# Performance work log

Measured on AMD Instinct MI355X. Metric: run time of the kernel, lower is better.

The kernel has to match this reference:

```python
import jax, jax.numpy as jnp
import numpy as np

D, NH, NL, NP, NLAYERS = 256, 8, 4, 4, 6
DH = D // NH
SHAPES = [(76, 100), (38, 50), (19, 25), (10, 13)]
STARTS = [int(s) for s in np.cumsum([0] + [h * w for h, w in SHAPES])[:-1]]
LQ = sum(h * w for h, w in SHAPES)
B = 2


def _layernorm(x, g, b, eps=1e-5):
    m = x.mean(-1, keepdims=True)
    v = ((x - m) ** 2).mean(-1, keepdims=True)
    return (x - m) * jax.lax.rsqrt(v + eps) * g + b


def _ref_points():
    pts = []
    for H, W in SHAPES:
        ry = (jnp.arange(H, dtype=jnp.float32) + 0.5) / H
        rx = (jnp.arange(W, dtype=jnp.float32) + 0.5) / W
        gy, gx = jnp.meshgrid(ry, rx, indexing='ij')
        pts.append(jnp.stack([gx.ravel(), gy.ravel()], -1))
    ref = jnp.concatenate(pts, 0)  # [LQ, 2] (x, y)
    return jnp.broadcast_to(ref[:, None, :], (LQ, NL, 2))


def _bilinear(v, loc, H, W):
    # v: [BN, H*W, DH]; loc: [BN, N, 2] normalized (x, y).
    # Matches torch grid_sample(align_corners=False, padding='zeros') with grid=2*loc-1.
    px = loc[..., 0] * W - 0.5
    py = loc[..., 1] * H - 0.5
    x0f = jnp.floor(px)
    y0f = jnp.floor(py)
    lx = px - x0f
    ly = py - y0f
    x0 = x0f.astype(jnp.int32)
    y0 = y0f.astype(jnp.int32)
    out = jnp.zeros(loc.shape[:-1] + (DH,), v.dtype)
    for dy, dx, w in ((0, 0, (1 - ly) * (1 - lx)), (0, 1, (1 - ly) * lx), (1, 0, ly * (1 - lx)), (1, 1, ly * lx)):
        xi = x0 + dx
        yi = y0 + dy
        valid = (xi >= 0) & (xi < W) & (yi >= 0) & (yi < H)
        idx = jnp.clip(yi, 0, H - 1) * W + jnp.clip(xi, 0, W - 1)
        g = jnp.take_along_axis(v, idx[..., None], axis=1)  # [BN, N, DH]
        out = out + g * (w * valid)[..., None]
    return out


def _layer(src, pos, ref, p):
    q = src + pos
    value = (src @ p['w_val'] + p['b_val']).reshape(B, LQ, NH, DH)
    off = (q @ p['w_off'] + p['b_off']).reshape(B, LQ, NH, NL, NP, 2)
    aw = jax.nn.softmax((q @ p['w_attn'] + p['b_attn']).reshape(B, LQ, NH, NL * NP), -1)
    aw = aw.reshape(B, LQ, NH, NL, NP)
    norm = jnp.array([[w, h] for h, w in SHAPES], jnp.float32)  # [NL, 2] = (W, H)
    loc = ref[None, :, None, :, None, :] + off / norm[None, None, None, :, None, :]  # [B,LQ,NH,NL,NP,2]
    v_t = value.transpose(0, 2, 1, 3).reshape(B * NH, LQ, DH)
    out = jnp.zeros((B, NH, LQ, DH), src.dtype)
    for l, (H, W) in enumerate(SHAPES):
        vl = v_t[:, STARTS[l]:STARTS[l] + H * W]
        locl = loc[:, :, :, l].transpose(0, 2, 1, 3, 4).reshape(B * NH, LQ * NP, 2)
        g = _bilinear(vl, locl, H, W).reshape(B, NH, LQ, NP, DH)
        out = out + jnp.einsum('bhqp,bhqpd->bhqd', aw[:, :, :, l].transpose(0, 2, 1, 3), g)
    attn = out.transpose(0, 2, 1, 3).reshape(B, LQ, D) @ p['w_out'] + p['b_out']
    src = _layernorm(src + attn, p['ln1_g'], p['ln1_b'])
    ffn = jax.nn.relu(src @ p['w_ffn1'] + p['b_ffn1']) @ p['w_ffn2'] + p['b_ffn2']
    return _layernorm(src + ffn, p['ln2_g'], p['ln2_b'])


def setup_inputs() -> dict:
    key = jax.random.key(0)
    ks = jax.random.split(key, 16)
    inp = {}
    for i, (H, W) in enumerate(SHAPES):
        inp[f'src{i}'] = jax.random.normal(ks[i], (B, D, H, W), jnp.float32)
        inp[f'pos{i}'] = jax.random.normal(ks[4 + i], (B, D, H, W), jnp.float32)
    inp['level_embed'] = jax.random.normal(ks[8], (NL, D), jnp.float32)
    s = 0.02
    inp['w_off'] = jax.random.normal(ks[9], (NLAYERS, D, NH * NL * NP * 2), jnp.float32) * s
    inp['b_off'] = jnp.zeros((NLAYERS, NH * NL * NP * 2), jnp.float32)
    inp['w_attn'] = jax.random.normal(ks[10], (NLAYERS, D, NH * NL * NP), jnp.float32) * s
    inp['b_attn'] = jnp.zeros((NLAYERS, NH * NL * NP), jnp.float32)
    inp['w_val'] = jax.random.normal(ks[11], (NLAYERS, D, D), jnp.float32) * s
    inp['b_val'] = jnp.zeros((NLAYERS, D), jnp.float32)
    inp['w_out'] = jax.random.normal(ks[12], (NLAYERS, D, D), jnp.float32) * s
    inp['b_out'] = jnp.zeros((NLAYERS, D), jnp.float32)
    inp['ln1_g'] = jnp.ones((NLAYERS, D), jnp.float32)
    inp['ln1_b'] = jnp.zeros((NLAYERS, D), jnp.float32)
    inp['w_ffn1'] = jax.random.normal(ks[13], (NLAYERS, D, 1024), jnp.float32) * s
    inp['b_ffn1'] = jnp.zeros((NLAYERS, 1024), jnp.float32)
    inp['w_ffn2'] = jax.random.normal(ks[14], (NLAYERS, 1024, D), jnp.float32) * s
    inp['b_ffn2'] = jnp.zeros((NLAYERS, D), jnp.float32)
    inp['ln2_g'] = jnp.ones((NLAYERS, D), jnp.float32)
    inp['ln2_b'] = jnp.zeros((NLAYERS, D), jnp.float32)
    return inp


def reference(src0, src1, src2, src3, pos0, pos1, pos2, pos3, level_embed,
              w_off, b_off, w_attn, b_attn, w_val, b_val, w_out, b_out,
              ln1_g, ln1_b, w_ffn1, b_ffn1, w_ffn2, b_ffn2, ln2_g, ln2_b):
    srcs = [src0, src1, src2, src3]
    poss = [pos0, pos1, pos2, pos3]
    src_flat = jnp.concatenate(
        [s.reshape(B, D, -1).transpose(0, 2, 1) + level_embed[l][None, None] for l, s in enumerate(srcs)], 1)
    pos_flat = jnp.concatenate([p.reshape(B, D, -1).transpose(0, 2, 1) for p in poss], 1)
    ref = _ref_points()
    x = src_flat
    for i in range(NLAYERS):
        p = dict(w_off=w_off[i], b_off=b_off[i], w_attn=w_attn[i], b_attn=b_attn[i],
                 w_val=w_val[i], b_val=b_val[i], w_out=w_out[i], b_out=b_out[i],
                 ln1_g=ln1_g[i], ln1_b=ln1_b[i], w_ffn1=w_ffn1[i], b_ffn1=b_ffn1[i],
                 w_ffn2=w_ffn2[i], b_ffn2=b_ffn2[i], ln2_g=ln2_g[i], ln2_b=ln2_b[i])
        x = _layer(x, pos_flat, ref, p)
    return x  # [B, LQ, D] encoded memory
```

## Files before the change

kernel.cpp:

```cpp
#include <hip/hip_runtime.h>
#include <math.h>

#define LQ 10105
#define BATCH 2
#define NLAYERS 6
#define NTOK (BATCH * LQ)

typedef __attribute__((ext_vector_type(8))) short bf16x8;
typedef __attribute__((ext_vector_type(4))) float f32x4;

__device__ inline unsigned short f2bf_rne(float f) {
    unsigned u = __float_as_uint(f);
    unsigned r = u + 0x7fffu + ((u >> 16) & 1u);
    return (unsigned short)(r >> 16);
}
__device__ inline float bf2f(unsigned short h) {
    return __uint_as_float((unsigned)h << 16);
}

__global__ __launch_bounds__(256)
void flatten_k(const float* __restrict__ src, const float* __restrict__ pos,
               const float* __restrict__ lvl, float* __restrict__ src_flat,
               float* __restrict__ pos_flat, int HW, int start)
{
    int hw = blockIdx.x;
    int b  = blockIdx.y;
    int d  = threadIdx.x;
    float sv = src[((size_t)b * 256 + d) * HW + hw];
    float pv = pos[((size_t)b * 256 + d) * HW + hw];
    size_t o = ((size_t)(b * LQ + start + hw)) * 256 + d;
    src_flat[o] = sv + lvl[d];
    pos_flat[o] = pv;
}

__global__ __launch_bounds__(256)
void wsplit_k(const float* __restrict__ W, unsigned short* __restrict__ Th,
              unsigned short* __restrict__ Tl, int K, int N,
              long srcStride, long dstStride)
{
    __shared__ float t[32][33];
    int layer = blockIdx.z;
    int n0 = blockIdx.x * 32, k0 = blockIdx.y * 32;
    int tx = threadIdx.x & 31, ty = threadIdx.x >> 5;
    const float* Wsrc = W + (size_t)layer * srcStride;
    #pragma unroll
    for (int i = 0; i < 4; ++i)
        t[ty + i * 8][tx] = Wsrc[(size_t)(k0 + ty + i * 8) * N + n0 + tx];
    __syncthreads();
    unsigned short* th = Th + (size_t)layer * dstStride;
    unsigned short* tl = Tl + (size_t)layer * dstStride;
    #pragma unroll
    for (int i = 0; i < 4; ++i) {
        int n = n0 + ty + i * 8;
        float v = t[tx][ty + i * 8];
        unsigned short h = f2bf_rne(v);
        th[(size_t)n * K + k0 + tx] = h;
        tl[(size_t)n * K + k0 + tx] = f2bf_rne(v - bf2f(h));
    }
}

__global__ void boa_k(const float* __restrict__ b_off,
                      const float* __restrict__ b_attn, float* __restrict__ boa)
{
    int l = blockIdx.x, t = threadIdx.x;
    boa[l * 384 + t] = (t < 256) ? b_off[l * 256 + t] : b_attn[l * 128 + (t - 256)];
}

template<bool A_BF16, bool HAS_A2, bool RELU, bool HAS_RES, bool C_BF16>
__global__ __launch_bounds__(256)
void gemm_mfma(const void* __restrict__ Av, const float* __restrict__ A2,
               const unsigned short* __restrict__ Bh,
               const unsigned short* __restrict__ Bl,
               const float* __restrict__ bias, const float* __restrict__ Res,
               void* __restrict__ Cv, int M, int N, int K, int NB)
{
    constexpr int LDR = 40;
    constexpr int PLANES = A_BF16 ? 3 : 4;
    __shared__ unsigned short sMem[PLANES * 128 * LDR];
    unsigned short* sBh = sMem;
    unsigned short* sBl = sMem + 128 * LDR;
    unsigned short* sAh = sMem + 2 * 128 * LDR;
    unsigned short* sAl = sMem + (PLANES - 1) * 128 * LDR;

    const int nwg = gridDim.x;
    const int bid = blockIdx.x;
    const int q8 = nwg >> 3, r8 = nwg & 7, xcd = bid & 7;
    const int work = (xcd < r8 ? xcd * (q8 + 1) : r8 * (q8 + 1) + (xcd - r8) * q8)
                     + (bid >> 3);
    const int mblk = work / NB;
    const int m0 = mblk * 128;
    const int n0 = (work - mblk * NB) * 128;

    const int tid = threadIdx.x;
    const int w  = tid >> 6;
    const int l  = tid & 63;
    const int wm = (w >> 1) * 64;
    const int wn = (w & 1) * 64;
    const int lr = l & 15;
    const int kb = (l >> 4) * 8;
    const int rr = (l >> 4) * 4;

    const int sm = tid >> 1;
    const int sk = (tid & 1) * 16;
    const int arow = m0 + sm;
    const bool aok = arow < M;

    f32x4 acc[4][4];
    #pragma unroll
    for (int i = 0; i < 4; ++i)
        #pragma unroll
        for (int j = 0; j < 4; ++j)
            acc[i][j] = (f32x4){0.f, 0.f, 0.f, 0.f};

    for (int kt = 0; kt < K; kt += 32) {
        const unsigned short* bph = &Bh[(size_t)(n0 + sm) * K + kt + sk];
        const unsigned short* bpl = &Bl[(size_t)(n0 + sm) * K + kt + sk];
        bf16x8 vbh0 = *(const bf16x8*)(bph);
        bf16x8 vbh1 = *(const bf16x8*)(bph + 8);
        bf16x8 vbl0 = *(const bf16x8*)(bpl);
        bf16x8 vbl1 = *(const bf16x8*)(bpl + 8);

        bf16x8 ah0 = {}, ah1 = {}, al0 = {}, al1 = {};
        if constexpr (A_BF16) {
            if (aok) {
                const unsigned short* ap =
                    (const unsigned short*)Av + (size_t)arow * K + kt + sk;
                ah0 = *(const bf16x8*)ap;
                ah1 = *(const bf16x8*)(ap + 8);
            }
        } else {
            float va[16];
            if (aok) {
                const float* ap = (const float*)Av + (size_t)arow * K + kt + sk;
                *(float4*)&va[0]  = *(const float4*)(ap + 0);
                *(float4*)&va[4]  = *(const float4*)(ap + 4);
                *(float4*)&va[8]  = *(const float4*)(ap + 8);
                *(float4*)&va[12] = *(const float4*)(ap + 12);
                if (HAS_A2) {
                    const float* ap2 = &A2[(size_t)arow * K + kt + sk];
                    float4 t0 = *(const float4*)(ap2 + 0);
                    float4 t1 = *(const float4*)(ap2 + 4);
                    float4 t2 = *(const float4*)(ap2 + 8);
                    float4 t3 = *(const float4*)(ap2 + 12);
                    va[0] += t0.x; va[1] += t0.y; va[2]  += t0.z; va[3]  += t0.w;
                    va[4] += t1.x; va[5] += t1.y; va[6]  += t1.z; va[7]  += t1.w;
                    va[8] += t2.x; va[9] += t2.y; va[10] += t2.z; va[11] += t2.w;
                    va[12]+= t3.x; va[13]+= t3.y; va[14] += t3.z; va[15] += t3.w;
                }
            } else {
                #pragma unroll
                for (int j = 0; j < 16; ++j) va[j] = 0.f;
            }
            #pragma unroll
            for (int j = 0; j < 8; ++j) {
                float v0 = va[j], v1 = va[8 + j];
                unsigned short h0 = (unsigned short)(__float_as_uint(v0) >> 16);
                unsigned short h1 = (unsigned short)(__float_as_uint(v1) >> 16);
                ah0[j] = (short)h0;
                ah1[j] = (short)h1;
                float r0 = v0 - bf2f(h0);
                float r1 = v1 - bf2f(h1);
                al0[j] = (short)(unsigned short)(__float_as_uint(r0) >> 16);
                al1[j] = (short)(unsigned short)(__float_as_uint(r1) >> 16);
            }
        }

        __syncthreads();
        *(bf16x8*)&sAh[sm * LDR + sk]     = ah0;
        *(bf16x8*)&sAh[sm * LDR + sk + 8] = ah1;
        if constexpr (!A_BF16) {
            *(bf16x8*)&sAl[sm * LDR + sk]     = al0;
            *(bf16x8*)&sAl[sm * LDR + sk + 8] = al1;
        }
        *(bf16x8*)&sBh[sm * LDR + sk]     = vbh0;
        *(bf16x8*)&sBh[sm * LDR + sk + 8] = vbh1;
        *(bf16x8*)&sBl[sm * LDR + sk]     = vbl0;
        *(bf16x8*)&sBl[sm * LDR + sk + 8] = vbl1;
        __syncthreads();

        bf16x8 fah[4], fal[4];
        #pragma unroll
        for (int mf = 0; mf < 4; ++mf) {
            int off = (wm + mf * 16 + lr) * LDR + kb;
            fah[mf] = *(const bf16x8*)&sAh[off];
            if constexpr (!A_BF16) fal[mf] = *(const bf16x8*)&sAl[off];
        }
        #pragma unroll
        for (int nf = 0; nf < 4; ++nf) {
            int boff = (wn + nf * 16 + lr) * LDR + kb;
            bf16x8 fbh = *(const bf16x8*)&sBh[boff];
            bf16x8 fbl = *(const bf16x8*)&sBl[boff];
            #pragma unroll
            for (int mf = 0; mf < 4; ++mf) {
                f32x4 c = acc[mf][nf];
                c = __builtin_amdgcn_mfma_f32_16x16x32_bf16(fah[mf], fbh, c, 0, 0, 0);
                c = __builtin_amdgcn_mfma_f32_16x16x32_bf16(fah[mf], fbl, c, 0, 0, 0);
                if constexpr (!A_BF16)
                    c = __builtin_amdgcn_mfma_f32_16x16x32_bf16(fal[mf], fbh, c, 0, 0, 0);
                acc[mf][nf] = c;
            }
        }
    }

    float* Cf = (float*)Cv;
    unsigned short* Cb = (unsigned short*)Cv;
    #pragma unroll
    for (int nf = 0; nf < 4; ++nf) {
        int col = n0 + wn + nf * 16 + lr;
        float bs = bias[col];
        #pragma unroll
        for (int mf = 0; mf < 4; ++mf) {
            int rowb = m0 + wm + mf * 16 + rr;
            #pragma unroll
            for (int r = 0; r < 4; ++r) {
                int row = rowb + r;
                if (row < M) {
                    float v = acc[mf][nf][r] + bs;
                    if (HAS_RES) v += Res[(size_t)row * N + col];
                    if (RELU) v = fmaxf(v, 0.f);
                    if constexpr (C_BF16)
                        Cb[(size_t)row * N + col] = f2bf_rne(v);
                    else
                        Cf[(size_t)row * N + col] = v;
                }
            }
        }
    }
}

__global__ __launch_bounds__(256)
void sample_k(const unsigned short* __restrict__ val,
              const float* __restrict__ oab, unsigned short* __restrict__ out)
{
    const int Hs[4] = {76, 38, 19, 10};
    const int Ws[4] = {100, 50, 25, 13};
    const int ST[4] = {0, 7600, 9500, 9975};

    int bid = blockIdx.x;
    int xcd = bid & 7;
    const int qch = LQ >> 3;
    const int rem = LQ & 7;
    int q = (xcd < rem ? xcd * (qch + 1) : rem * (qch + 1) + (xcd - rem) * qch)
            + (bid >> 3);
    int b = blockIdx.y;
    int tid = threadIdx.x;

    __shared__ int2 s_iw[512];

    if (tid < 128) {
        int h = tid >> 4, pt = tid & 15, lvl = pt >> 2, p = pt & 3;
        int lq, local;
        if (q < 7600)      { lq = 0; local = q; }
        else if (q < 9500) { lq = 1; local = q - 7600; }
        else if (q < 9975) { lq = 2; local = q - 9500; }
        else               { lq = 3; local = q - 9975; }
        int Wq = Ws[lq], Hq = Hs[lq];
        int ry = local / Wq, rx = local - ry * Wq;
        float refx = (rx + 0.5f) / (float)Wq;
        float refy = (ry + 0.5f) / (float)Hq;

        size_t rowb = (size_t)(b * LQ + q) * 384;
        float logit = oab[rowb + 256 + h * 16 + pt];
        float mx = logit;
        mx = fmaxf(mx, __shfl_xor(mx, 1, 64));
        mx = fmaxf(mx, __shfl_xor(mx, 2, 64));
        mx = fmaxf(mx, __shfl_xor(mx, 4, 64));
        mx = fmaxf(mx, __shfl_xor(mx, 8, 64));
        float e = expf(logit - mx);
        float s = e;
        s += __shfl_xor(s, 1, 64);
        s += __shfl_xor(s, 2, 64);
        s += __shfl_xor(s, 4, 64);
        s += __shfl_xor(s, 8, 64);
        float aw = e / s;

        float ox = oab[rowb + h * 32 + lvl * 8 + p * 2];
        float oy = oab[rowb + h * 32 + lvl * 8 + p * 2 + 1];
        int W = Ws[lvl], H = Hs[lvl], st = ST[lvl];
        float px = refx * (float)W + ox - 0.5f;
        float py = refy * (float)H + oy - 0.5f;
        float x0f = floorf(px), y0f = floorf(py);
        float lx = px - x0f, ly = py - y0f;
        int x0 = (int)x0f, y0 = (int)y0f;
        int x1 = x0 + 1, y1 = y0 + 1;
        float ax0 = ((x0 >= 0) & (x0 < W)) ? (1.f - lx) : 0.f;
        float ax1 = ((x1 >= 0) & (x1 < W)) ? lx : 0.f;
        float ay0 = ((y0 >= 0) & (y0 < H)) ? (1.f - ly) : 0.f;
        float ay1 = ((y1 >= 0) & (y1 < H)) ? ly : 0.f;
        int cx0 = min(max(x0, 0), W - 1), cx1 = min(max(x1, 0), W - 1);
        int cy0 = min(max(y0, 0), H - 1), cy1 = min(max(y1, 0), H - 1);
        int i00 = st + cy0 * W + cx0, i01 = st + cy0 * W + cx1;
        int i10 = st + cy1 * W + cx0, i11 = st + cy1 * W + cx1;
        int base4 = tid * 4;
        s_iw[base4 + 0] = make_int2(i00, __float_as_int(aw * ay0 * ax0));
        s_iw[base4 + 1] = make_int2(i01, __float_as_int(aw * ay0 * ax1));
        s_iw[base4 + 2] = make_int2(i10, __float_as_int(aw * ay1 * ax0));
        s_iw[base4 + 3] = make_int2(i11, __float_as_int(aw * ay1 * ax1));
    }
    __syncthreads();

    int lane   = tid & 63;
    int wv     = tid >> 6;
    int h      = wv * 2 + (lane >> 5);
    int half   = lane & 31;
    int corner = half >> 3;
    int c4     = half & 7;
    const unsigned short* vb = val + (size_t)(b * LQ) * 256 + h * 32 + c4 * 4;
    int sbase = h * 64 + corner;

    float4 acc = make_float4(0.f, 0.f, 0.f, 0.f);
    #pragma unroll
    for (int pt = 0; pt < 16; ++pt) {
        int2 iw = s_iw[sbase + pt * 4];
        float wgt = __int_as_float(iw.y);
        ushort4 v = *(const ushort4*)&vb[(size_t)iw.x * 256];
        acc.x += wgt * bf2f(v.x); acc.y += wgt * bf2f(v.y);
        acc.z += wgt * bf2f(v.z); acc.w += wgt * bf2f(v.w);
    }
    acc.x += __shfl_xor(acc.x, 8, 64);  acc.y += __shfl_xor(acc.y, 8, 64);
    acc.z += __shfl_xor(acc.z, 8, 64);  acc.w += __shfl_xor(acc.w, 8, 64);
    acc.x += __shfl_xor(acc.x, 16, 64); acc.y += __shfl_xor(acc.y, 16, 64);
    acc.z += __shfl_xor(acc.z, 16, 64); acc.w += __shfl_xor(acc.w, 16, 64);

    if (corner == 0) {
        ushort4 o;
        o.x = f2bf_rne(acc.x); o.y = f2bf_rne(acc.y);
        o.z = f2bf_rne(acc.z); o.w = f2bf_rne(acc.w);
        *(ushort4*)&out[(size_t)(b * LQ + q) * 256 + h * 32 + c4 * 4] = o;
    }
}

__global__ __launch_bounds__(256)
void ln_k(const float* __restrict__ x, const float* __restrict__ g,
          const float* __restrict__ bt, float* __restrict__ out, int nrows)
{
    int row = blockIdx.x * 4 + (threadIdx.x >> 6);
    int lane = threadIdx.x & 63;
    if (row >= nrows) return;

    float4 v = *(const float4*)&x[(size_t)row * 256 + lane * 4];
    float s = v.x + v.y + v.z + v.w;
    #pragma unroll
    for (int o = 32; o > 0; o >>= 1) s += __shfl_down(s, o, 64);
    s = __shfl(s, 0, 64);
    float m = s * (1.0f / 256.0f);
    float cx = v.x - m, cy = v.y - m, cz = v.z - m, cw = v.w - m;
    float s2 = cx * cx + cy * cy + cz * cz + cw * cw;
    #pragma unroll
    for (int o = 32; o > 0; o >>= 1) s2 += __shfl_down(s2, o, 64);
    s2 = __shfl(s2, 0, 64);
    float rstd = rsqrtf(s2 * (1.0f / 256.0f) + 1e-5f);

    float4 gv = *(const float4*)&g[lane * 4];
    float4 bv = *(const float4*)&bt[lane * 4];
    float4 r;
    r.x = cx * rstd * gv.x + bv.x;
    r.y = cy * rstd * gv.y + bv.y;
    r.z = cz * rstd * gv.z + bv.z;
    r.w = cw * rstd * gv.w + bv.w;
    *(float4*)&out[(size_t)row * 256 + lane * 4] = r;
}

extern "C" void kernel_launch(void* const* d_in, const int* in_sizes, int n_in,
                              void* d_out, int out_size, void* d_ws, size_t ws_size,
                              hipStream_t stream)
{
    const float* src_in[4] = {(const float*)d_in[0], (const float*)d_in[2],
                              (const float*)d_in[4], (const float*)d_in[6]};
    const float* pos_in[4] = {(const float*)d_in[1], (const float*)d_in[3],
                              (const float*)d_in[5], (const float*)d_in[7]};
    const float* lvl    = (const float*)d_in[8];
    const float* w_off  = (const float*)d_in[9];
    const float* b_off  = (const float*)d_in[10];
    const float* w_attn = (const float*)d_in[11];
    const float* b_attn = (const float*)d_in[12];
    const float* w_val  = (const float*)d_in[13];
    const float* b_val  = (const float*)d_in[14];
    const float* w_out  = (const float*)d_in[15];
    const float* b_out  = (const float*)d_in[16];
    const float* ln1_g  = (const float*)d_in[17];
    const float* ln1_b  = (const float*)d_in[18];
    const float* w_ffn1 = (const float*)d_in[19];
    const float* b_ffn1 = (const float*)d_in[20];
    const float* w_ffn2 = (const float*)d_in[21];
    const float* b_ffn2 = (const float*)d_in[22];
    const float* ln2_g  = (const float*)d_in[23];
    const float* ln2_b  = (const float*)d_in[24];

    float* ws    = (float*)d_ws;
    float* src   = ws;
    float* pos   = src   + (size_t)NTOK * 256;
    float* preln = pos   + (size_t)NTOK * 256;
    char*  uni   = (char*)(preln + (size_t)NTOK * 256);
    unsigned short* valb = (unsigned short*)uni;
    float* oab = (float*)(uni + (size_t)NTOK * 512);
    unsigned short* samp = (unsigned short*)(uni + (size_t)NTOK * 2048);
    unsigned short* ffnb = (unsigned short*)uni;
    float* boa = (float*)(uni + (size_t)NTOK * 2560);
    unsigned short* Wh = (unsigned short*)(boa + 6 * 384);
    const long WL = 753664;
    unsigned short* Wl = Wh + (size_t)NLAYERS * WL;
    const long O_VAL = 0, O_OFF = 65536, O_ATT = 131072, O_OUT = 163840,
               O_F1 = 229376, O_F2 = 491520;

    wsplit_k<<<dim3(8, 8, 6),  256, 0, stream>>>(w_val,  Wh + O_VAL, Wl + O_VAL, 256, 256,  65536, WL);
    wsplit_k<<<dim3(8, 8, 6),  256, 0, stream>>>(w_off,  Wh + O_OFF, Wl + O_OFF, 256, 256,  65536, WL);
    wsplit_k<<<dim3(4, 8, 6),  256, 0, stream>>>(w_attn, Wh + O_ATT, Wl + O_ATT, 256, 128,  32768, WL);
    wsplit_k<<<dim3(8, 8, 6),  256, 0, stream>>>(w_out,  Wh + O_OUT, Wl + O_OUT, 256, 256,  65536, WL);
    wsplit_k<<<dim3(32, 8, 6), 256, 0, stream>>>(w_ffn1, Wh + O_F1,  Wl + O_F1,  256, 1024, 262144, WL);
    wsplit_k<<<dim3(8, 32, 6), 256, 0, stream>>>(w_ffn2, Wh + O_F2,  Wl + O_F2,  1024, 256, 262144, WL);
    boa_k<<<dim3(6), dim3(384), 0, stream>>>(b_off, b_attn, boa);

    const int HWs[4] = {7600, 1900, 475, 130};
    const int STt[4] = {0, 7600, 9500, 9975};
    for (int l = 0; l < 4; ++l) {
        dim3 g(HWs[l], BATCH);
        flatten_k<<<g, 256, 0, stream>>>(src_in[l], pos_in[l], lvl + l * 256,
                                         src, pos, HWs[l], STt[l]);
    }

    const int MB = (NTOK + 127) / 128;
    const int LNB = (NTOK + 3) / 4;
    dim3 blk(256);

    for (int i = 0; i < NLAYERS; ++i) {
        const unsigned short* whL = Wh + (size_t)i * WL;
        const unsigned short* wlL = Wl + (size_t)i * WL;
        const float* bv  = b_val  + (size_t)i * 256;
        const float* bou = b_out  + (size_t)i * 256;
        const float* l1g = ln1_g  + (size_t)i * 256;
        const float* l1b = ln1_b  + (size_t)i * 256;
        const float* bf1 = b_ffn1 + (size_t)i * 1024;
        const float* bf2 = b_ffn2 + (size_t)i * 256;
        const float* l2g = ln2_g  + (size_t)i * 256;
        const float* l2b = ln2_b  + (size_t)i * 256;

        gemm_mfma<false, false, false, false, true><<<dim3(MB * 2), blk, 0, stream>>>(
            src, nullptr, whL + O_VAL, wlL + O_VAL, bv, nullptr, valb, NTOK, 256, 256, 2);
        gemm_mfma<false, true, false, false, false><<<dim3(MB * 3), blk, 0, stream>>>(
            src, pos, whL + O_OFF, wlL + O_OFF, boa + (size_t)i * 384, nullptr,
            oab, NTOK, 384, 256, 3);
        sample_k<<<dim3(LQ, BATCH), blk, 0, stream>>>(valb, oab, samp);
        gemm_mfma<true, false, false, true, false><<<dim3(MB * 2), blk, 0, stream>>>(
            samp, nullptr, whL + O_OUT, wlL + O_OUT, bou, src, preln, NTOK, 256, 256, 2);
        ln_k<<<dim3(LNB), blk, 0, stream>>>(preln, l1g, l1b, src, NTOK);
        gemm_mfma<false, false, true, false, true><<<dim3(MB * 8), blk, 0, stream>>>(
            src, nullptr, whL + O_F1, wlL + O_F1, bf1, nullptr, ffnb, NTOK, 1024, 256, 8);
        gemm_mfma<true, false, false, true, false><<<dim3(MB * 2), blk, 0, stream>>>(
            ffnb, nullptr, whL + O_F2, wlL + O_F2, bf2, src, preln, NTOK, 256, 1024, 2);
        float* dst = (i == NLAYERS - 1) ? (float*)d_out : src;
        ln_k<<<dim3(LNB), blk, 0, stream>>>(preln, l2g, l2b, dst, NTOK);
    }
}
```

Baseline: 1.756 ms.

## Pre-split activations into bf16 planes in LN/flatten, fuse value+offset GEMMs, use direct global-to-LDS loads

```diff
diff --git a/kernel.cpp b/kernel.cpp
--- a/kernel.cpp
+++ b/kernel.cpp
@@ -17,20 +17,69 @@
 __device__ inline float bf2f(unsigned short h) {
     return __uint_as_float((unsigned)h << 16);
 }
+__device__ inline void split2(float v, unsigned short& h, unsigned short& l) {
+    h = (unsigned short)(__float_as_uint(v) >> 16);
+    float r = v - bf2f(h);
+    l = (unsigned short)(__float_as_uint(r) >> 16);
+}
+
+__device__ inline void stage_plane(const unsigned short* __restrict__ gp,
+                                   unsigned short* lp, int row0, int K, int kt,
+                                   int tid)
+{
+    int r  = row0 + (tid >> 2);
+    int kk = kt + (tid & 3) * 8;
+    __builtin_amdgcn_global_load_lds(
+        (const __attribute__((address_space(1))) void*)(gp + (size_t)r * K + kk),
+        (__attribute__((address_space(3))) void*)(lp + tid * 8), 16, 0, 0);
+    __builtin_amdgcn_global_load_lds(
+        (const __attribute__((address_space(1))) void*)(gp + (size_t)(r + 64) * K + kk),
+        (__attribute__((address_space(3))) void*)(lp + 2048 + tid * 8), 16, 0, 0);
+}
 
 __global__ __launch_bounds__(256)
 void flatten_k(const float* __restrict__ src, const float* __restrict__ pos,
-               const float* __restrict__ lvl, float* __restrict__ src_flat,
-               float* __restrict__ pos_flat, int HW, int start)
-{
-    int hw = blockIdx.x;
-    int b  = blockIdx.y;
-    int d  = threadIdx.x;
-    float sv = src[((size_t)b * 256 + d) * HW + hw];
-    float pv = pos[((size_t)b * 256 + d) * HW + hw];
-    size_t o = ((size_t)(b * LQ + start + hw)) * 256 + d;
-    src_flat[o] = sv + lvl[d];
-    pos_flat[o] = pv;
+               const float* __restrict__ lvl, float* __restrict__ srcf,
+               float* __restrict__ posf, unsigned short* __restrict__ sh,
+               unsigned short* __restrict__ sl, unsigned short* __restrict__ qh,
+               unsigned short* __restrict__ ql, int HW, int start)
+{
+    __shared__ float ts[64][65], tp[64][65];
+    int hw0 = blockIdx.x * 64;
+    int d0  = blockIdx.y * 64;
+    int b   = blockIdx.z;
+    int tid = threadIdx.x;
+    int c = tid & 63, rg = tid >> 6;
+
+    #pragma unroll 4
+    for (int i = 0; i < 16; ++i) {
+        int dl = rg * 16 + i;
+        int hw = hw0 + c;
+        float s = 0.f, p = 0.f;
+        if (hw < HW) {
+            s = src[(size_t)(b * 256 + d0 + dl) * HW + hw];
+            p = pos[(size_t)(b * 256 + d0 + dl) * HW + hw];
+        }
+        ts[dl][c] = s;
+        tp[dl][c] = p;
+    }
+    __syncthreads();
+    float lv = lvl[d0 + c];
+    #pragma unroll 4
+    for (int i = 0; i < 16; ++i) {
+        int hwl = rg * 16 + i;
+        int hw = hw0 + hwl;
+        if (hw >= HW) continue;
+        float s = ts[c][hwl] + lv;
+        float p = tp[c][hwl];
+        size_t o = (size_t)(b * LQ + start + hw) * 256 + d0 + c;
+        srcf[o] = s;
+        posf[o] = p;
+        unsigned short h, l;
+        split2(s, h, l); sh[o] = h; sl[o] = l;
+        float q = s + p;
+        split2(q, h, l); qh[o] = h; ql[o] = l;
+    }
 }
 
 __global__ __launch_bounds__(256)
@@ -59,135 +108,73 @@
     }
 }
 
-__global__ void boa_k(const float* __restrict__ b_off,
-                      const float* __restrict__ b_attn, float* __restrict__ boa)
+__global__ void boa_k(const float* __restrict__ b_val,
+                      const float* __restrict__ b_off,
+                      const float* __restrict__ b_attn, float* __restrict__ bo)
 {
     int l = blockIdx.x, t = threadIdx.x;
-    boa[l * 384 + t] = (t < 256) ? b_off[l * 256 + t] : b_attn[l * 128 + (t - 256)];
-}
-
-template<bool A_BF16, bool HAS_A2, bool RELU, bool HAS_RES, bool C_BF16>
+    float v;
+    if (t < 256)      v = b_val[l * 256 + t];
+    else if (t < 512) v = b_off[l * 256 + (t - 256)];
+    else              v = b_attn[l * 128 + (t - 512)];
+    bo[l * 640 + t] = v;
+}
+
 __global__ __launch_bounds__(256)
-void gemm_mfma(const void* __restrict__ Av, const float* __restrict__ A2,
-               const unsigned short* __restrict__ Bh,
-               const unsigned short* __restrict__ Bl,
-               const float* __restrict__ bias, const float* __restrict__ Res,
-               void* __restrict__ Cv, int M, int N, int K, int NB)
-{
-    constexpr int LDR = 40;
-    constexpr int PLANES = A_BF16 ? 3 : 4;
-    __shared__ unsigned short sMem[PLANES * 128 * LDR];
-    unsigned short* sBh = sMem;
-    unsigned short* sBl = sMem + 128 * LDR;
-    unsigned short* sAh = sMem + 2 * 128 * LDR;
-    unsigned short* sAl = sMem + (PLANES - 1) * 128 * LDR;
-
-    const int nwg = gridDim.x;
-    const int bid = blockIdx.x;
+void gemm_top(const unsigned short* __restrict__ Ash,
+              const unsigned short* __restrict__ Asl,
+              const unsigned short* __restrict__ Aqh,
+              const unsigned short* __restrict__ Aql,
+              const unsigned short* __restrict__ Bh,
+              const unsigned short* __restrict__ Bl,
+              const float* __restrict__ bias640,
+              unsigned short* __restrict__ valb, float* __restrict__ oab, int M)
+{
+    constexpr int K = 256, NB = 5;
+    __shared__ unsigned short sP[4 * 4096];
+    unsigned short* sAh = sP;
+    unsigned short* sAl = sP + 4096;
+    unsigned short* sBh = sP + 8192;
+    unsigned short* sBl = sP + 12288;
+
+    const int nwg = gridDim.x, bid = blockIdx.x;
     const int q8 = nwg >> 3, r8 = nwg & 7, xcd = bid & 7;
     const int work = (xcd < r8 ? xcd * (q8 + 1) : r8 * (q8 + 1) + (xcd - r8) * q8)
                      + (bid >> 3);
     const int mblk = work / NB;
-    const int m0 = mblk * 128;
-    const int n0 = (work - mblk * NB) * 128;
+    const int nb = work - mblk * NB;
+    const int m0 = mblk * 128, n0 = nb * 128;
+
+    const unsigned short* Ah = (nb < 2) ? Ash : Aqh;
+    const unsigned short* Al = (nb < 2) ? Asl : Aql;
 
     const int tid = threadIdx.x;
-    const int w  = tid >> 6;
-    const int l  = tid & 63;
-    const int wm = (w >> 1) * 64;
-    const int wn = (w & 1) * 64;
-    const int lr = l & 15;
-    const int kb = (l >> 4) * 8;
-    const int rr = (l >> 4) * 4;
-
-    const int sm = tid >> 1;
-    const int sk = (tid & 1) * 16;
-    const int arow = m0 + sm;
-    const bool aok = arow < M;
+    const int w = tid >> 6, l = tid & 63;
+    const int wm = (w >> 1) * 64, wn = (w & 1) * 64;
+    const int lr = l & 15, kb = (l >> 4) * 8, rr = (l >> 4) * 4;
 
     f32x4 acc[4][4];
     #pragma unroll
     for (int i = 0; i < 4; ++i)
         #pragma unroll
-        for (int j = 0; j < 4; ++j)
-            acc[i][j] = (f32x4){0.f, 0.f, 0.f, 0.f};
+        for (int j = 0; j < 4; ++j) acc[i][j] = (f32x4){0.f, 0.f, 0.f, 0.f};
 
     for (int kt = 0; kt < K; kt += 32) {
-        const unsigned short* bph = &Bh[(size_t)(n0 + sm) * K + kt + sk];
-        const unsigned short* bpl = &Bl[(size_t)(n0 + sm) * K + kt + sk];
-        bf16x8 vbh0 = *(const bf16x8*)(bph);
-        bf16x8 vbh1 = *(const bf16x8*)(bph + 8);
-        bf16x8 vbl0 = *(const bf16x8*)(bpl);
-        bf16x8 vbl1 = *(const bf16x8*)(bpl + 8);
-
-        bf16x8 ah0 = {}, ah1 = {}, al0 = {}, al1 = {};
-        if constexpr (A_BF16) {
-            if (aok) {
-                const unsigned short* ap =
-                    (const unsigned short*)Av + (size_t)arow * K + kt + sk;
-                ah0 = *(const bf16x8*)ap;
-                ah1 = *(const bf16x8*)(ap + 8);
-            }
-        } else {
-            float va[16];
-            if (aok) {
-                const float* ap = (const float*)Av + (size_t)arow * K + kt + sk;
-                *(float4*)&va[0]  = *(const float4*)(ap + 0);
-                *(float4*)&va[4]  = *(const float4*)(ap + 4);
-                *(float4*)&va[8]  = *(const float4*)(ap + 8);
-                *(float4*)&va[12] = *(const float4*)(ap + 12);
-                if (HAS_A2) {
-                    const float* ap2 = &A2[(size_t)arow * K + kt + sk];
-                    float4 t0 = *(const float4*)(ap2 + 0);
-                    float4 t1 = *(const float4*)(ap2 + 4);
-                    float4 t2 = *(const float4*)(ap2 + 8);
-                    float4 t3 = *(const float4*)(ap2 + 12);
-                    va[0] += t0.x; va[1] += t0.y; va[2]  += t0.z; va[3]  += t0.w;
-                    va[4] += t1.x; va[5] += t1.y; va[6]  += t1.z; va[7]  += t1.w;
-                    va[8] += t2.x; va[9] += t2.y; va[10] += t2.z; va[11] += t2.w;
-                    va[12]+= t3.x; va[13]+= t3.y; va[14] += t3.z; va[15] += t3.w;
-                }
-            } else {
-                #pragma unroll
-                for (int j = 0; j < 16; ++j) va[j] = 0.f;
-            }
-            #pragma unroll
-            for (int j = 0; j < 8; ++j) {
-                float v0 = va[j], v1 = va[8 + j];
-                unsigned short h0 = (unsigned short)(__float_as_uint(v0) >> 16);
-                unsigned short h1 = (unsigned short)(__float_as_uint(v1) >> 16);
-                ah0[j] = (short)h0;
-                ah1[j] = (short)h1;
-                float r0 = v0 - bf2f(h0);
-                float r1 = v1 - bf2f(h1);
-                al0[j] = (short)(unsigned short)(__float_as_uint(r0) >> 16);
-                al1[j] = (short)(unsigned short)(__float_as_uint(r1) >> 16);
-            }
-        }
-
+        stage_plane(Ah, sAh, m0, K, kt, tid);
+        stage_plane(Al, sAl, m0, K, kt, tid);
+        stage_plane(Bh, sBh, n0, K, kt, tid);
+        stage_plane(Bl, sBl, n0, K, kt, tid);
         __syncthreads();
-        *(bf16x8*)&sAh[sm * LDR + sk]     = ah0;
-        *(bf16x8*)&sAh[sm * LDR + sk + 8] = ah1;
-        if constexpr (!A_BF16) {
-            *(bf16x8*)&sAl[sm * LDR + sk]     = al0;
-            *(bf16x8*)&sAl[sm * LDR + sk + 8] = al1;
-        }
-        *(bf16x8*)&sBh[sm * LDR + sk]     = vbh0;
-        *(bf16x8*)&sBh[sm * LDR + sk + 8] = vbh1;
-        *(bf16x8*)&sBl[sm * LDR + sk]     = vbl0;
-        *(bf16x8*)&sBl[sm * LDR + sk + 8] = vbl1;
-        __syncthreads();
-
         bf16x8 fah[4], fal[4];
         #pragma unroll
         for (int mf = 0; mf < 4; ++mf) {
-            int off = (wm + mf * 16 + lr) * LDR + kb;
+            int off = (wm + mf * 16 + lr) * 32 + kb;
             fah[mf] = *(const bf16x8*)&sAh[off];
-            if constexpr (!A_BF16) fal[mf] = *(const bf16x8*)&sAl[off];
+            fal[mf] = *(const bf16x8*)&sAl[off];
         }
         #pragma unroll
         for (int nf = 0; nf < 4; ++nf) {
-            int boff = (wn + nf * 16 + lr) * LDR + kb;
+            int boff = (wn + nf * 16 + lr) * 32 + kb;
             bf16x8 fbh = *(const bf16x8*)&sBh[boff];
             bf16x8 fbl = *(const bf16x8*)&sBl[boff];
             #pragma unroll
@@ -195,19 +182,17 @@
                 f32x4 c = acc[mf][nf];
                 c = __builtin_amdgcn_mfma_f32_16x16x32_bf16(fah[mf], fbh, c, 0, 0, 0);
                 c = __builtin_amdgcn_mfma_f32_16x16x32_bf16(fah[mf], fbl, c, 0, 0, 0);
-                if constexpr (!A_BF16)
-                    c = __builtin_amdgcn_mfma_f32_16x16x32_bf16(fal[mf], fbh, c, 0, 0, 0);
+                c = __builtin_amdgcn_mfma_f32_16x16x32_bf16(fal[mf], fbh, c, 0, 0, 0);
                 acc[mf][nf] = c;
             }
         }
-    }
-
-    float* Cf = (float*)Cv;
-    unsigned short* Cb = (unsigned short*)Cv;
+        __syncthreads();
+    }
+
     #pragma unroll
     for (int nf = 0; nf < 4; ++nf) {
-        int col = n0 + wn + nf * 16 + lr;
-        float bs = bias[col];
+        int ncol = n0 + wn + nf * 16 + lr;
+        float bs = bias640[ncol];
         #pragma unroll
         for (int mf = 0; mf < 4; ++mf) {
             int rowb = m0 + wm + mf * 16 + rr;
@@ -216,12 +201,97 @@
                 int row = rowb + r;
                 if (row < M) {
                     float v = acc[mf][nf][r] + bs;
-                    if (HAS_RES) v += Res[(size_t)row * N + col];
+                    if (nb < 2) valb[(size_t)row * 256 + ncol] = f2bf_rne(v);
+                    else        oab[(size_t)row * 384 + (ncol - 256)] = v;
+                }
+            }
+        }
+    }
+}
+
+template<int PASSES, bool RELU, bool HAS_RES, bool C_BF16>
+__global__ __launch_bounds__(256)
+void gemm_std(const unsigned short* __restrict__ Ah,
+              const unsigned short* __restrict__ Al,
+              const unsigned short* __restrict__ Bh,
+              const unsigned short* __restrict__ Bl,
+              const float* __restrict__ bias, const float* __restrict__ Res,
+              void* __restrict__ Cv, int M, int N, int K, int NB)
+{
+    __shared__ unsigned short sP[(PASSES + 1) * 4096];
+    unsigned short* sAh = sP;
+    unsigned short* sAl = sP + 4096;
+    unsigned short* sBh = sP + (PASSES - 1) * 4096;
+    unsigned short* sBl = sP + PASSES * 4096;
+
+    const int nwg = gridDim.x, bid = blockIdx.x;
+    const int q8 = nwg >> 3, r8 = nwg & 7, xcd = bid & 7;
+    const int work = (xcd < r8 ? xcd * (q8 + 1) : r8 * (q8 + 1) + (xcd - r8) * q8)
+                     + (bid >> 3);
+    const int mblk = work / NB;
+    const int m0 = mblk * 128;
+    const int n0 = (work - mblk * NB) * 128;
+
+    const int tid = threadIdx.x;
+    const int w = tid >> 6, l = tid & 63;
+    const int wm = (w >> 1) * 64, wn = (w & 1) * 64;
+    const int lr = l & 15, kb = (l >> 4) * 8, rr = (l >> 4) * 4;
+
+    f32x4 acc[4][4];
+    #pragma unroll
+    for (int i = 0; i < 4; ++i)
+        #pragma unroll
+        for (int j = 0; j < 4; ++j) acc[i][j] = (f32x4){0.f, 0.f, 0.f, 0.f};
+
+    for (int kt = 0; kt < K; kt += 32) {
+        stage_plane(Ah, sAh, m0, K, kt, tid);
+        if (PASSES == 3) stage_plane(Al, sAl, m0, K, kt, tid);
+        stage_plane(Bh, sBh, n0, K, kt, tid);
+        stage_plane(Bl, sBl, n0, K, kt, tid);
+        __syncthreads();
+        bf16x8 fah[4], fal[4];
+        #pragma unroll
+        for (int mf = 0; mf < 4; ++mf) {
+            int off = (wm + mf * 16 + lr) * 32 + kb;
+            fah[mf] = *(const bf16x8*)&sAh[off];
+            if (PASSES == 3) fal[mf] = *(const bf16x8*)&sAl[off];
+        }
+        #pragma unroll
+        for (int nf = 0; nf < 4; ++nf) {
+            int boff = (wn + nf * 16 + lr) * 32 + kb;
+            bf16x8 fbh = *(const bf16x8*)&sBh[boff];
+            bf16x8 fbl = *(const bf16x8*)&sBl[boff];
+            #pragma unroll
+            for (int mf = 0; mf < 4; ++mf) {
+                f32x4 c = acc[mf][nf];
+                c = __builtin_amdgcn_mfma_f32_16x16x32_bf16(fah[mf], fbh, c, 0, 0, 0);
+                c = __builtin_amdgcn_mfma_f32_16x16x32_bf16(fah[mf], fbl, c, 0, 0, 0);
+                if (PASSES == 3)
+                    c = __builtin_amdgcn_mfma_f32_16x16x32_bf16(fal[mf], fbh, c, 0, 0, 0);
+                acc[mf][nf] = c;
+            }
+        }
+        __syncthreads();
+    }
+
+    float* Cf = (float*)Cv;
+    unsigned short* Cb = (unsigned short*)Cv;
+    #pragma unroll
+    for (int nf = 0; nf < 4; ++nf) {
+        int ncol = n0 + wn + nf * 16 + lr;
+        float bs = bias[ncol];
+        #pragma unroll
+        for (int mf = 0; mf < 4; ++mf) {
+            int rowb = m0 + wm + mf * 16 + rr;
+            #pragma unroll
+            for (int r = 0; r < 4; ++r) {
+                int row = rowb + r;
+                if (row < M) {
+                    float v = acc[mf][nf][r] + bs;
+                    if (HAS_RES) v += Res[(size_t)row * N + ncol];
                     if (RELU) v = fmaxf(v, 0.f);
-                    if constexpr (C_BF16)
-                        Cb[(size_t)row * N + col] = f2bf_rne(v);
-                    else
-                        Cf[(size_t)row * N + col] = v;
+                    if (C_BF16) Cb[(size_t)row * N + ncol] = f2bf_rne(v);
+                    else        Cf[(size_t)row * N + ncol] = v;
                 }
             }
         }
@@ -330,9 +400,13 @@
     }
 }
 
+template<bool EMIT_Q, bool EMIT_PLANES>
 __global__ __launch_bounds__(256)
-void ln_k(const float* __restrict__ x, const float* __restrict__ g,
-          const float* __restrict__ bt, float* __restrict__ out, int nrows)
+void ln_plane_k(const float* __restrict__ x, const float* __restrict__ g,
+                const float* __restrict__ bt, const float* __restrict__ pos,
+                float* __restrict__ dst, unsigned short* __restrict__ sh,
+                unsigned short* __restrict__ sl, unsigned short* __restrict__ qh,
+                unsigned short* __restrict__ ql, int nrows)
 {
     int row = blockIdx.x * 4 + (threadIdx.x >> 6);
     int lane = threadIdx.x & 63;
@@ -358,7 +432,24 @@
     r.y = cy * rstd * gv.y + bv.y;
     r.z = cz * rstd * gv.z + bv.z;
     r.w = cw * rstd * gv.w + bv.w;
-    *(float4*)&out[(size_t)row * 256 + lane * 4] = r;
+    size_t o4 = (size_t)row * 256 + lane * 4;
+    *(float4*)&dst[o4] = r;
+
+    if (EMIT_PLANES) {
+        ushort4 hh, ll;
+        split2(r.x, hh.x, ll.x); split2(r.y, hh.y, ll.y);
+        split2(r.z, hh.z, ll.z); split2(r.w, hh.w, ll.w);
+        *(ushort4*)&sh[o4] = hh;
+        *(ushort4*)&sl[o4] = ll;
+    }
+    if (EMIT_Q) {
+        float4 pv = *(const float4*)&pos[o4];
+        ushort4 hh, ll;
+        split2(r.x + pv.x, hh.x, ll.x); split2(r.y + pv.y, hh.y, ll.y);
+        split2(r.z + pv.z, hh.z, ll.z); split2(r.w + pv.w, hh.w, ll.w);
+        *(ushort4*)&qh[o4] = hh;
+        *(ushort4*)&ql[o4] = ll;
+    }
 }
 
 extern "C" void kernel_launch(void* const* d_in, const int* in_sizes, int n_in,
@@ -387,17 +478,21 @@
     const float* ln2_g  = (const float*)d_in[23];
     const float* ln2_b  = (const float*)d_in[24];
 
-    float* ws    = (float*)d_ws;
-    float* src   = ws;
-    float* pos   = src   + (size_t)NTOK * 256;
-    float* preln = pos   + (size_t)NTOK * 256;
-    char*  uni   = (char*)(preln + (size_t)NTOK * 256);
+    char* wsb = (char*)d_ws;
+    float* src  = (float*)wsb;
+    float* pos  = src + (size_t)NTOK * 256;
+    float* preln = pos + (size_t)NTOK * 256;
+    unsigned short* sh = (unsigned short*)(preln + (size_t)NTOK * 256);
+    unsigned short* sl = sh + (size_t)NTOK * 256;
+    unsigned short* qh = sl + (size_t)NTOK * 256;
+    unsigned short* ql = qh + (size_t)NTOK * 256;
+    char* uni = (char*)(ql + (size_t)NTOK * 256);
     unsigned short* valb = (unsigned short*)uni;
     float* oab = (float*)(uni + (size_t)NTOK * 512);
     unsigned short* samp = (unsigned short*)(uni + (size_t)NTOK * 2048);
     unsigned short* ffnb = (unsigned short*)uni;
-    float* boa = (float*)(uni + (size_t)NTOK * 2560);
-    unsigned short* Wh = (unsigned short*)(boa + 6 * 384);
+    float* boa640 = (float*)(uni + (size_t)NTOK * 2560);
+    unsigned short* Wh = (unsigned short*)(boa640 + 6 * 640);
     const long WL = 753664;
     unsigned short* Wl = Wh + (size_t)NLAYERS * WL;
     const long O_VAL = 0, O_OFF = 65536, O_ATT = 131072, O_OUT = 163840,
@@ -409,14 +504,14 @@
     wsplit_k<<<dim3(8, 8, 6),  256, 0, stream>>>(w_out,  Wh + O_OUT, Wl + O_OUT, 256, 256,  65536, WL);
     wsplit_k<<<dim3(32, 8, 6), 256, 0, stream>>>(w_ffn1, Wh + O_F1,  Wl + O_F1,  256, 1024, 262144, WL);
     wsplit_k<<<dim3(8, 32, 6), 256, 0, stream>>>(w_ffn2, Wh + O_F2,  Wl + O_F2,  1024, 256, 262144, WL);
-    boa_k<<<dim3(6), dim3(384), 0, stream>>>(b_off, b_attn, boa);
+    boa_k<<<dim3(6), dim3(640), 0, stream>>>(b_val, b_off, b_attn, boa640);
 
     const int HWs[4] = {7600, 1900, 475, 130};
     const int STt[4] = {0, 7600, 9500, 9975};
     for (int l = 0; l < 4; ++l) {
-        dim3 g(HWs[l], BATCH);
+        dim3 g((HWs[l] + 63) / 64, 4, BATCH);
         flatten_k<<<g, 256, 0, stream>>>(src_in[l], pos_in[l], lvl + l * 256,
-                                         src, pos, HWs[l], STt[l]);
+                                         src, pos, sh, sl, qh, ql, HWs[l], STt[l]);
     }
 
     const int MB = (NTOK + 127) / 128;
@@ -426,7 +521,6 @@
     for (int i = 0; i < NLAYERS; ++i) {
         const unsigned short* whL = Wh + (size_t)i * WL;
         const unsigned short* wlL = Wl + (size_t)i * WL;
-        const float* bv  = b_val  + (size_t)i * 256;
         const float* bou = b_out  + (size_t)i * 256;
         const float* l1g = ln1_g  + (size_t)i * 256;
         const float* l1b = ln1_b  + (size_t)i * 256;
@@ -435,20 +529,26 @@
         const float* l2g = ln2_g  + (size_t)i * 256;
         const float* l2b = ln2_b  + (size_t)i * 256;
 
-        gemm_mfma<false, false, false, false, true><<<dim3(MB * 2), blk, 0, stream>>>(
-            src, nullptr, whL + O_VAL, wlL + O_VAL, bv, nullptr, valb, NTOK, 256, 256, 2);
-        gemm_mfma<false, true, false, false, false><<<dim3(MB * 3), blk, 0, stream>>>(
-            src, pos, whL + O_OFF, wlL + O_OFF, boa + (size_t)i * 384, nullptr,
-            oab, NTOK, 384, 256, 3);
+        gemm_top<<<dim3(MB * 5), blk, 0, stream>>>(
+            sh, sl, qh, ql, whL, wlL, boa640 + (size_t)i * 640, valb, oab, NTOK);
         sample_k<<<dim3(LQ, BATCH), blk, 0, stream>>>(valb, oab, samp);
-        gemm_mfma<true, false, false, true, false><<<dim3(MB * 2), blk, 0, stream>>>(
-            samp, nullptr, whL + O_OUT, wlL + O_OUT, bou, src, preln, NTOK, 256, 256, 2);
-        ln_k<<<dim3(LNB), blk, 0, stream>>>(preln, l1g, l1b, src, NTOK);
-        gemm_mfma<false, false, true, false, true><<<dim3(MB * 8), blk, 0, stream>>>(
-            src, nullptr, whL + O_F1, wlL + O_F1, bf1, nullptr, ffnb, NTOK, 1024, 256, 8);
-        gemm_mfma<true, false, false, true, false><<<dim3(MB * 2), blk, 0, stream>>>(
-            ffnb, nullptr, whL + O_F2, wlL + O_F2, bf2, src, preln, NTOK, 256, 1024, 2);
-        float* dst = (i == NLAYERS - 1) ? (float*)d_out : src;
-        ln_k<<<dim3(LNB), blk, 0, stream>>>(preln, l2g, l2b, dst, NTOK);
-    }
-}
+        gemm_std<2, false, true, false><<<dim3(MB * 2), blk, 0, stream>>>(
+            samp, nullptr, whL + O_OUT, wlL + O_OUT, bou, src, preln,
+            NTOK, 256, 256, 2);
+        ln_plane_k<false, true><<<dim3(LNB), blk, 0, stream>>>(
+            preln, l1g, l1b, nullptr, src, sh, sl, nullptr, nullptr, NTOK);
+        gemm_std<3, true, false, true><<<dim3(MB * 8), blk, 0, stream>>>(
+            sh, sl, whL + O_F1, wlL + O_F1, bf1, nullptr, ffnb,
+            NTOK, 1024, 256, 8);
+        gemm_std<2, false, true, false><<<dim3(MB * 2), blk, 0, stream>>>(
+            ffnb, nullptr, whL + O_F2, wlL + O_F2, bf2, src, preln,
+            NTOK, 256, 1024, 2);
+        if (i == NLAYERS - 1)
+            ln_plane_k<false, false><<<dim3(LNB), blk, 0, stream>>>(
+                preln, l2g, l2b, nullptr, (float*)d_out,
+                nullptr, nullptr, nullptr, nullptr, NTOK);
+        else
+            ln_plane_k<true, true><<<dim3(LNB), blk, 0, stream>>>(
+                preln, l2g, l2b, pos, src, sh, sl, qh, ql, NTOK);
+    }
+}
```

Measured after the change: 1.792 ms. 2.0% more time.
